# Optimization experiments

Measured on AMD Instinct MI355X. Metric: run time of the kernel, lower is better.

Reference implementation:

```python
import jax, jax.numpy as jnp
import numpy as np

D_MODEL = 1024
N_HEADS = 16
HEAD_DIM = D_MODEL // N_HEADS


def setup_inputs() -> dict:
    key = jax.random.key(0)
    k1, k2, k3 = jax.random.split(key, 3)
    x = jax.random.normal(k1, (2, 2048, D_MODEL), dtype=jnp.float32)
    w_qkv = jax.random.normal(k2, (3 * D_MODEL, D_MODEL), dtype=jnp.float32) * 0.02
    w_out = jax.random.normal(k3, (D_MODEL, D_MODEL), dtype=jnp.float32) * 0.02
    return {"x": x, "w_qkv": w_qkv, "w_out": w_out}


def reference(x, w_qkv, w_out):
    B, T, D = x.shape
    H, Hd = N_HEADS, HEAD_DIM
    # QKV projection: Linear stores weight as [out, in] -> '...i,oi->...o'
    qkv = jnp.einsum('bti,oi->bto', x, w_qkv)              # [B, T, 3D]
    # split (3*H, Hs) group-major, chunk into q/k/v of H heads each
    qkv = qkv.reshape(B, T, 3, H, Hd)
    q = jnp.transpose(qkv[:, :, 0], (0, 2, 1, 3))          # [B, H, T, Hd]
    k = jnp.transpose(qkv[:, :, 1], (0, 2, 1, 3))
    v = jnp.transpose(qkv[:, :, 2], (0, 2, 1, 3))
    scale = 1.0 / jnp.sqrt(jnp.asarray(Hd, dtype=x.dtype))
    scores = jnp.einsum('bhqd,bhkd->bhqk', q, k) * scale   # [B, H, T, T]
    causal = jnp.tril(jnp.ones((T, T), dtype=bool))        # [T, T]
    scores = jnp.where(causal[None, None], scores, jnp.asarray(-jnp.inf, dtype=scores.dtype))
    attn = jax.nn.softmax(scores, axis=-1)
    ctx = jnp.einsum('bhqk,bhkd->bhqd', attn, v)           # [B, H, T, Hd]
    ctx = jnp.transpose(ctx, (0, 2, 1, 3)).reshape(B, T, D)
    return jnp.einsum('bti,oi->bto', ctx, w_out)
```

## Files before the change

### kernel.cpp

```cpp
#include <hip/hip_runtime.h>


typedef short short8 __attribute__((ext_vector_type(8)));
typedef float f32x4 __attribute__((ext_vector_type(4)));
typedef unsigned short u16;
typedef unsigned int u32;

#define T_SEQ 2048
#define N_B 2
#define N_H 16
#define HD 64
#define DM 1024
#define TRIPLE 3072

__device__ __forceinline__ u16 f2bf(float f) {
  union { float f; unsigned u; } v;
  v.f = f;
  unsigned r = v.u + 0x7fffu + ((v.u >> 16) & 1u);
  return (u16)(r >> 16);
}

__device__ __forceinline__ float bf2f(u16 x) {
  return __uint_as_float((u32)x << 16);
}

__device__ __forceinline__ u32 cvtpk(float a, float b) {
  u32 r;
  asm("v_cvt_pk_bf16_f32 %0, %1, %2" : "=v"(r) : "v"(a), "v"(b));
  return r;
}

typedef const __attribute__((address_space(1))) void gvoid;
typedef __attribute__((address_space(3))) void lvoid;

__device__ __forceinline__ void g2l16(const void* g, void* l) {
  __builtin_amdgcn_global_load_lds((gvoid*)g, (lvoid*)l, 16, 0, 0);
}

__device__ __forceinline__ void storeC(float* p, float v) { *p = v; }
__device__ __forceinline__ void storeC(u16* p, float v) { *p = f2bf(v); }

__global__ __launch_bounds__(256) void cast_all(const float4* __restrict__ x,
                                                const float4* __restrict__ wq,
                                                const float4* __restrict__ wo,
                                                ushort4* __restrict__ out) {
  int i = blockIdx.x * 256 + threadIdx.x;
  const float4* src;
  int off;
  if (i < 1048576) { src = x; off = 0; }
  else if (i < 1835008) { src = wq; off = 1048576; }
  else { src = wo; off = 1835008; }
  float4 v = src[i - off];
  ushort4 o;
  o.x = f2bf(v.x); o.y = f2bf(v.y); o.z = f2bf(v.z); o.w = f2bf(v.w);
  out[i] = o;
}

__global__ __launch_bounds__(256) void vtrans(const u16* __restrict__ qkv,
                                              u16* __restrict__ vT) {
  const int tid = threadIdx.x;
  const int w = tid >> 6, lane = tid & 63;
  const int ti = lane >> 3, di = lane & 7;
  const int h = blockIdx.y, b = blockIdx.z;
  const int t0 = blockIdx.x * 256 + w * 64 + ti * 8;

  const u16* src = qkv + (size_t)(b * T_SEQ + t0) * TRIPLE + 2 * DM + h * HD + di * 8;
  u32 x[8][4];
#pragma unroll
  for (int e = 0; e < 8; ++e) {
    union { short8 v; u32 u[4]; } cv;
    cv.v = *(const short8*)(src + (size_t)e * TRIPLE);
#pragma unroll
    for (int j = 0; j < 4; ++j) x[e][j] = cv.u[j];
  }
  u32 y[8][4];
#pragma unroll
  for (int a = 0; a < 4; ++a)
#pragma unroll
    for (int j = 0; j < 4; ++j) {
      u32 lo = x[2 * a][j], hi = x[2 * a + 1][j];
      y[2 * a][j] = (lo & 0x0000FFFFu) | (hi << 16);
      y[2 * a + 1][j] = (lo >> 16) | (hi & 0xFFFF0000u);
    }
  u16* dst = vT + ((size_t)(b * N_H + h) * HD + di * 8) * T_SEQ + t0;
#pragma unroll
  for (int dd = 0; dd < 8; ++dd) {
    union { short8 v; u32 u[4]; } cv;
#pragma unroll
    for (int a = 0; a < 4; ++a) cv.u[a] = y[2 * a + (dd & 1)][dd >> 1];
    *(short8*)(dst + (size_t)dd * T_SEQ) = cv.v;
  }
}

template <typename OutT>
__global__ __launch_bounds__(512, 2) void gemm_bt_256(const u16* __restrict__ A,
                                                      const u16* __restrict__ W,
                                                      OutT* __restrict__ C,
                                                      int M, int N, int K) {
  __shared__ char As[2][32768];
  __shared__ char Bs[2][32768];

  const int tid = threadIdx.x;
  const int lane = tid & 63, w = tid >> 6;
  const int l15 = lane & 15, l4 = lane >> 4;
  const int wm = w >> 2, wn = w & 3;
  const int m0 = blockIdx.y * 256, n0 = blockIdx.x * 256;

  const int srow = tid >> 3;
  const int sswz = ((tid & 7) ^ (srow & 7)) << 3;
  const u16* Abase = A + (size_t)(m0 + srow) * K + sswz;
  const u16* Bbase = W + (size_t)(n0 + srow) * K + sswz;

  const f32x4 zero = {0.f, 0.f, 0.f, 0.f};
  f32x4 acc[8][4];
#pragma unroll
  for (int am = 0; am < 8; ++am)
#pragma unroll
    for (int n = 0; n < 4; ++n) acc[am][n] = zero;

#define STAGE8(k0_, buf_)                                                      \
  {                                                                            \
    _Pragma("unroll") for (int r_ = 0; r_ < 4; ++r_) {                         \
      g2l16(Abase + (size_t)(64 * r_) * K + (k0_),                             \
            As[buf_] + (r_ * 512 + tid) * 16);                                 \
      g2l16(Bbase + (size_t)(64 * r_) * K + (k0_),                             \
            Bs[buf_] + (r_ * 512 + tid) * 16);                                 \
    }                                                                          \
  }

  STAGE8(0, 0);

  const int nkt = K >> 6;
  for (int kt = 0;; ++kt) {
    const int cur = kt & 1;

    if (kt + 1 < nkt) {
      STAGE8((kt + 1) << 6, cur ^ 1);
      asm volatile("s_waitcnt vmcnt(8)" ::: "memory");
    } else {
      asm volatile("s_waitcnt vmcnt(0)" ::: "memory");
    }
    __builtin_amdgcn_s_barrier();

#pragma unroll
    for (int ph = 0; ph < 4; ++ph) {
      const int kk = ph >> 1, mh = ph & 1;
      short8 a[4], b[4];
#pragma unroll
      for (int m = 0; m < 4; ++m) {
        int row = wm * 128 + mh * 64 + m * 16 + l15;
        int slot = (kk * 4 + l4) ^ (row & 7);
        a[m] = *(const short8*)(As[cur] + row * 128 + slot * 16);
      }
#pragma unroll
      for (int n = 0; n < 4; ++n) {
        int row = wn * 64 + n * 16 + l15;
        int slot = (kk * 4 + l4) ^ (row & 7);
        b[n] = *(const short8*)(Bs[cur] + row * 128 + slot * 16);
      }
      asm volatile("s_waitcnt lgkmcnt(0)" ::: "memory");
      __builtin_amdgcn_s_setprio(1);
#pragma unroll
      for (int m = 0; m < 4; ++m)
#pragma unroll
        for (int n = 0; n < 4; ++n)
          acc[mh * 4 + m][n] =
              __builtin_amdgcn_mfma_f32_16x16x32_bf16(a[m], b[n], acc[mh * 4 + m][n], 0, 0, 0);
      __builtin_amdgcn_s_setprio(0);
    }

    if (kt + 1 >= nkt) break;
    __builtin_amdgcn_s_barrier();
  }
#undef STAGE8

#pragma unroll
  for (int am = 0; am < 8; ++am)
#pragma unroll
    for (int n = 0; n < 4; ++n)
#pragma unroll
      for (int r = 0; r < 4; ++r) {
        int row = m0 + wm * 128 + (am >> 2) * 64 + (am & 3) * 16 + l4 * 4 + r;
        int col = n0 + wn * 64 + n * 16 + l15;
        storeC(C + (size_t)row * N + col, acc[am][n][r]);
      }
}

template <typename OutT>
__global__ __launch_bounds__(256) void gemm_bt(const u16* __restrict__ A,
                                               const u16* __restrict__ W,
                                               OutT* __restrict__ C,
                                               int M, int N, int K) {
  __shared__ char As[128 * 64 * 2];
  __shared__ char Bs[128 * 64 * 2];
  const int tid = threadIdx.x;
  const int lane = tid & 63, w = tid >> 6;
  const int l15 = lane & 15, l4 = lane >> 4;
  const int m0 = blockIdx.y * 128, n0 = blockIdx.x * 128;
  const int wr = (w >> 1) * 64, wc = (w & 1) * 64;

  const f32x4 zero = {0.f, 0.f, 0.f, 0.f};
  f32x4 acc[4][4];
#pragma unroll
  for (int m = 0; m < 4; ++m)
#pragma unroll
    for (int n = 0; n < 4; ++n) acc[m][n] = zero;

  for (int k0 = 0; k0 < K; k0 += 64) {
#pragma unroll
    for (int i = 0; i < 4; ++i) {
      const int cb = (i * 4 + w) * 64;
      const int c = cb + lane;
      const int row = c >> 3;
      const int ks = ((c & 7) ^ (row & 7)) * 8;
      g2l16(A + (size_t)(m0 + row) * K + k0 + ks, As + (size_t)cb * 16);
      g2l16(W + (size_t)(n0 + row) * K + k0 + ks, Bs + (size_t)cb * 16);
    }
    __syncthreads();

#pragma unroll
    for (int kk = 0; kk < 2; ++kk) {
      short8 a[4], b[4];
#pragma unroll
      for (int m = 0; m < 4; ++m) {
        int row = wr + m * 16 + l15;
        int slot = (kk * 4 + l4) ^ (row & 7);
        a[m] = *(const short8*)(As + row * 128 + slot * 16);
      }
#pragma unroll
      for (int n = 0; n < 4; ++n) {
        int row = wc + n * 16 + l15;
        int slot = (kk * 4 + l4) ^ (row & 7);
        b[n] = *(const short8*)(Bs + row * 128 + slot * 16);
      }
#pragma unroll
      for (int m = 0; m < 4; ++m)
#pragma unroll
        for (int n = 0; n < 4; ++n)
          acc[m][n] = __builtin_amdgcn_mfma_f32_16x16x32_bf16(a[m], b[n], acc[m][n], 0, 0, 0);
    }
    __syncthreads();
  }

#pragma unroll
  for (int m = 0; m < 4; ++m)
#pragma unroll
    for (int n = 0; n < 4; ++n)
#pragma unroll
      for (int r = 0; r < 4; ++r) {
        int row = m0 + wr + m * 16 + l4 * 4 + r;
        int col = n0 + wc + n * 16 + l15;
        storeC(C + (size_t)row * N + col, acc[m][n][r]);
      }
}

__global__ __launch_bounds__(512) void attn_fwd(const u16* __restrict__ qkv,
                                                const u16* __restrict__ vT,
                                                u16* __restrict__ ctx) {
  __shared__ char Ks[3][8192];
  __shared__ char Vs[3][8192];
  __shared__ char Pl[8][2048];

  const int tid = threadIdx.x;
  const int lane = tid & 63, w = tid >> 6;
  const int l15 = lane & 15, l4 = lane >> 4;
  const int g = blockIdx.x;
  const int p = blockIdx.y;
  const int h = g & 15, b = g >> 4;
  const int q0A = 128 * p, q0B = 128 * (15 - p);
  const int nA = 2 * p + 2;

  const float c_log2 = 0.18033688011112042f;
  short8 qa2[2][2];
#pragma unroll
  for (int ps = 0; ps < 2; ++ps) {
    const int qq0 = ps ? q0B : q0A;
    const u16* qp = qkv + (size_t)(b * T_SEQ + qq0 + w * 16 + l15) * TRIPLE + h * HD;
#pragma unroll
    for (int kk = 0; kk < 2; ++kk) {
      short8 raw = *(const short8*)(qp + kk * 32 + l4 * 8);
      union { short8 v; u32 w4[4]; } qq;
#pragma unroll
      for (int j = 0; j < 4; ++j)
        qq.w4[j] = cvtpk(bf2f((u16)raw[2 * j]) * c_log2,
                         bf2f((u16)raw[2 * j + 1]) * c_log2);
      qa2[ps][kk] = qq.v;
    }
  }

  const int r0 = tid >> 3, c0 = tid & 7;
  const int swz = (c0 ^ (r0 & 7)) << 3;
  const u16* kbase = qkv + (size_t)(b * T_SEQ + r0) * TRIPLE + DM + h * HD + swz;
  const u16* vbase = vT + ((size_t)g * HD + r0) * T_SEQ + swz;

#define STAGE(kt_, buf_)                                                     \
  {                                                                          \
    g2l16(kbase + (size_t)((kt_) * (64 * TRIPLE)), Ks[buf_] + tid * 16);     \
    g2l16(vbase + (u32)((kt_) * 64), Vs[buf_] + tid * 16);                   \
  }

  char* Plb = Pl[w];

  const f32x4 zero = {0.f, 0.f, 0.f, 0.f};
  f32x4 o[4];
#pragma unroll
  for (int nt = 0; nt < 4; ++nt) o[nt] = zero;
  float mr = -INFINITY, lr = 0.f;
  short8 qa0 = qa2[0][0], qa1 = qa2[0][1];
  int q0 = q0A;

  STAGE(0, 0);
  STAGE(1, 1);
  asm volatile("s_waitcnt vmcnt(2)\n\ts_barrier" ::: "memory");

  int cur = 0;
  for (int i = 0;; ++i) {
    const int kt = (i < nA) ? i : 33 - i;

    if (i + 2 < 34) {
      const int kt2 = (i + 2 < nA) ? (i + 2) : 31 - i;
      int sb = cur - 1;
      if (sb < 0) sb = 2;
      STAGE(kt2, sb);
    }

    const int k0 = kt * 64;
    if (k0 <= q0 + w * 16) {
      f32x4 s[4];
#pragma unroll
      for (int mt = 0; mt < 4; ++mt) s[mt] = zero;
      __builtin_amdgcn_s_setprio(1);
#pragma unroll
      for (int mt = 0; mt < 4; ++mt) {
        int row = mt * 16 + l15;
        int slot0 = l4 ^ (row & 7);
        short8 kb0 = *(const short8*)(Ks[cur] + row * 128 + slot0 * 16);
        s[mt] = __builtin_amdgcn_mfma_f32_16x16x32_bf16(kb0, qa0, s[mt], 0, 0, 0);
        int slot1 = (4 + l4) ^ (row & 7);
        short8 kb1 = *(const short8*)(Ks[cur] + row * 128 + slot1 * 16);
        s[mt] = __builtin_amdgcn_mfma_f32_16x16x32_bf16(kb1, qa1, s[mt], 0, 0, 0);
      }
      __builtin_amdgcn_s_setprio(0);

      if (i >= nA - 2 && i <= nA + 1) {
        const int qrow = q0 + w * 16 + l15;
#pragma unroll
        for (int mt = 0; mt < 4; ++mt)
#pragma unroll
          for (int r = 0; r < 4; ++r) {
            int key = k0 + mt * 16 + l4 * 4 + r;
            if (key > qrow) s[mt][r] = -INFINITY;
          }
      }

      float mx = fmaxf(fmaxf(fmaxf(s[0][0], s[0][1]), fmaxf(s[0][2], s[0][3])),
                       fmaxf(fmaxf(s[1][0], s[1][1]), fmaxf(s[1][2], s[1][3])));
      mx = fmaxf(mx, fmaxf(fmaxf(fmaxf(s[2][0], s[2][1]), fmaxf(s[2][2], s[2][3])),
                           fmaxf(fmaxf(s[3][0], s[3][1]), fmaxf(s[3][2], s[3][3]))));
      mx = fmaxf(mx, __shfl_xor(mx, 16));
      mx = fmaxf(mx, __shfl_xor(mx, 32));
      if (!__all(mx - mr <= 8.0f)) {
        float mn = fmaxf(mr, mx);
        float fr = exp2f(mr - mn);
        lr *= fr;
#pragma unroll
        for (int r = 0; r < 4; ++r) {
          float frq = __shfl(fr, l4 * 4 + r);
#pragma unroll
          for (int nt = 0; nt < 4; ++nt) o[nt][r] *= frq;
        }
        mr = mn;
      }
      float ps = 0.f;
#pragma unroll
      for (int mt = 0; mt < 4; ++mt)
#pragma unroll
        for (int r = 0; r < 4; ++r) {
          float pv = exp2f(s[mt][r] - mr);
          s[mt][r] = pv;
          ps += pv;
        }
      lr += ps;

#pragma unroll
      for (int mt = 0; mt < 4; ++mt) {
        uint2 pw;
        pw.x = cvtpk(s[mt][0], s[mt][1]);
        pw.y = cvtpk(s[mt][2], s[mt][3]);
        int slot = ((mt * 2 + (l4 >> 1)) ^ (l15 & 7));
        *(uint2*)(Plb + l15 * 128 + (slot << 4) + ((l4 & 1) << 3)) = pw;
      }

      __builtin_amdgcn_s_setprio(1);
#pragma unroll
      for (int kk = 0; kk < 2; ++kk) {
        short8 pa = *(const short8*)(Plb + l15 * 128 + (((kk * 4 + l4) ^ (l15 & 7)) << 4));
#pragma unroll
        for (int nt = 0; nt < 4; ++nt) {
          int d = nt * 16 + l15;
          int slot = (kk * 4 + l4) ^ (l15 & 7);
          short8 vb = *(const short8*)(Vs[cur] + d * 128 + slot * 16);
          o[nt] = __builtin_amdgcn_mfma_f32_16x16x32_bf16(pa, vb, o[nt], 0, 0, 0);
        }
      }
      __builtin_amdgcn_s_setprio(0);
    }

    if (i == nA - 1 || i == 33) {
      lr += __shfl_xor(lr, 16);
      lr += __shfl_xor(lr, 32);
#pragma unroll
      for (int r = 0; r < 4; ++r) {
        float lrq = __shfl(lr, l4 * 4 + r);
        float inv = __builtin_amdgcn_rcpf(lrq);
        size_t t = (size_t)(b * T_SEQ + q0 + w * 16 + l4 * 4 + r);
#pragma unroll
        for (int nt = 0; nt < 4; ++nt)
          ctx[t * DM + h * HD + nt * 16 + l15] = f2bf(o[nt][r] * inv);
      }
      if (i == 33) break;
#pragma unroll
      for (int nt = 0; nt < 4; ++nt) o[nt] = zero;
      mr = -INFINITY; lr = 0.f;
      qa0 = qa2[1][0]; qa1 = qa2[1][1];
      q0 = q0B;
    }

    if (i == 32)
      asm volatile("s_waitcnt vmcnt(0)\n\ts_barrier" ::: "memory");
    else
      asm volatile("s_waitcnt vmcnt(2)\n\ts_barrier" ::: "memory");
    cur = (cur == 2) ? 0 : cur + 1;
  }
#undef STAGE
}

extern "C" void kernel_launch(void* const* d_in, const int* in_sizes, int n_in,
                              void* d_out, int out_size, void* d_ws, size_t ws_size,
                              hipStream_t stream) {
  const float* x = (const float*)d_in[0];
  const float* wqkv = (const float*)d_in[1];
  const float* wout = (const float*)d_in[2];
  float* out = (float*)d_out;
  char* ws = (char*)d_ws;

  u16* xb    = (u16*)(ws);
  u16* wqkvb = (u16*)(ws + 8u * 1024 * 1024);
  u16* woutb = (u16*)(ws + 14u * 1024 * 1024);
  u16* qkvb  = (u16*)(ws + 16u * 1024 * 1024);
  u16* ctxb  = (u16*)(ws + 40u * 1024 * 1024);
  u16* vTb   = (u16*)(ws + 48u * 1024 * 1024);

  cast_all<<<8192, 256, 0, stream>>>((const float4*)x, (const float4*)wqkv,
                                     (const float4*)wout, (ushort4*)xb);

  gemm_bt_256<u16><<<dim3(12, 16), 512, 0, stream>>>(xb, wqkvb, qkvb, 4096, 3072, 1024);

  vtrans<<<dim3(8, N_H, N_B), 256, 0, stream>>>(qkvb, vTb);

  attn_fwd<<<dim3(32, 8), 512, 0, stream>>>(qkvb, vTb, ctxb);

  gemm_bt<float><<<dim3(8, 32), 256, 0, stream>>>(ctxb, woutb, out, 4096, 1024, 1024);
}
```

Baseline: 129.9 us.

## Split GEMM K-tile into half-stages interleaved with MFMA phases

Reorganizes the 256x256 GEMM's shared-memory staging into four half-tiles (A/B × two K halves of 32), each loaded with a new XOR swizzle. The next tile's loads are issued piecewise inside each MFMA phase, with a finer-grained vmcnt wait and a barrier per phase. The aim is to spread global-to-LDS traffic across the compute phases instead of issuing it all in one burst. It adds two barriers per phase, which raises sync overhead, and it relies on a new swizzle whose bank-conflict behavior is unverified.

```diff
diff --git a/kernel.cpp b/kernel.cpp
--- a/kernel.cpp
+++ b/kernel.cpp
@@ -97,8 +97,7 @@
                                                       const u16* __restrict__ W,
                                                       OutT* __restrict__ C,
                                                       int M, int N, int K) {
-  __shared__ char As[2][32768];
-  __shared__ char Bs[2][32768];
+  __shared__ char Ls[2][2][2][16384];
 
   const int tid = threadIdx.x;
   const int lane = tid & 63, w = tid >> 6;
@@ -106,10 +105,26 @@
   const int wm = w >> 2, wn = w & 3;
   const int m0 = blockIdx.y * 256, n0 = blockIdx.x * 256;
 
-  const int srow = tid >> 3;
-  const int sswz = ((tid & 7) ^ (srow & 7)) << 3;
-  const u16* Abase = A + (size_t)(m0 + srow) * K + sswz;
-  const u16* Bbase = W + (size_t)(n0 + srow) * K + sswz;
+  const int c0 = tid, c1 = 512 + tid;
+  const int r0 = c0 >> 2, r1 = c1 >> 2;
+  const int k0off = ((c0 & 3) ^ (((r0 >> 1) ^ (r0 >> 3)) & 3)) << 3;
+  const int k1off = ((c1 & 3) ^ (((r1 >> 1) ^ (r1 >> 3)) & 3)) << 3;
+  const u16* A0 = A + (size_t)(m0 + r0) * K + k0off;
+  const u16* A1 = A + (size_t)(m0 + r1) * K + k1off;
+  const u16* B0 = W + (size_t)(n0 + r0) * K + k0off;
+  const u16* B1 = W + (size_t)(n0 + r1) * K + k1off;
+
+#define STAGEH(mat_, kh_, kt_, buf_)                                           \
+  {                                                                            \
+    const int ko_ = (kt_) * 64 + (kh_) * 32;                                   \
+    if ((mat_) == 0) {                                                         \
+      g2l16(A0 + ko_, Ls[buf_][0][kh_] + tid * 16);                            \
+      g2l16(A1 + ko_, Ls[buf_][0][kh_] + (512 + tid) * 16);                    \
+    } else {                                                                   \
+      g2l16(B0 + ko_, Ls[buf_][1][kh_] + tid * 16);                            \
+      g2l16(B1 + ko_, Ls[buf_][1][kh_] + (512 + tid) * 16);                    \
+    }                                                                          \
+  }
 
   const f32x4 zero = {0.f, 0.f, 0.f, 0.f};
   f32x4 acc[8][4];
@@ -118,47 +133,47 @@
 #pragma unroll
     for (int n = 0; n < 4; ++n) acc[am][n] = zero;
 
-#define STAGE8(k0_, buf_)                                                      \
-  {                                                                            \
-    _Pragma("unroll") for (int r_ = 0; r_ < 4; ++r_) {                         \
-      g2l16(Abase + (size_t)(64 * r_) * K + (k0_),                             \
-            As[buf_] + (r_ * 512 + tid) * 16);                                 \
-      g2l16(Bbase + (size_t)(64 * r_) * K + (k0_),                             \
-            Bs[buf_] + (r_ * 512 + tid) * 16);                                 \
-    }                                                                          \
-  }
-
-  STAGE8(0, 0);
-
   const int nkt = K >> 6;
-  for (int kt = 0;; ++kt) {
+
+  STAGEH(0, 0, 0, 0);
+  STAGEH(1, 0, 0, 0);
+  STAGEH(0, 1, 0, 0);
+  STAGEH(1, 1, 0, 0);
+  asm volatile("s_waitcnt vmcnt(4)" ::: "memory");
+  __builtin_amdgcn_s_barrier();
+
+  for (int kt = 0; kt < nkt; ++kt) {
     const int cur = kt & 1;
-
-    if (kt + 1 < nkt) {
-      STAGE8((kt + 1) << 6, cur ^ 1);
-      asm volatile("s_waitcnt vmcnt(8)" ::: "memory");
-    } else {
-      asm volatile("s_waitcnt vmcnt(0)" ::: "memory");
-    }
-    __builtin_amdgcn_s_barrier();
+    const bool notlast = (kt + 1 < nkt);
 
 #pragma unroll
     for (int ph = 0; ph < 4; ++ph) {
       const int kk = ph >> 1, mh = ph & 1;
+
       short8 a[4], b[4];
 #pragma unroll
       for (int m = 0; m < 4; ++m) {
         int row = wm * 128 + mh * 64 + m * 16 + l15;
-        int slot = (kk * 4 + l4) ^ (row & 7);
-        a[m] = *(const short8*)(As[cur] + row * 128 + slot * 16);
+        int slot = l4 ^ (((row >> 1) ^ (row >> 3)) & 3);
+        a[m] = *(const short8*)(Ls[cur][0][kk] + row * 64 + (slot << 4));
       }
 #pragma unroll
       for (int n = 0; n < 4; ++n) {
         int row = wn * 64 + n * 16 + l15;
-        int slot = (kk * 4 + l4) ^ (row & 7);
-        b[n] = *(const short8*)(Bs[cur] + row * 128 + slot * 16);
-      }
+        int slot = l4 ^ (((row >> 1) ^ (row >> 3)) & 3);
+        b[n] = *(const short8*)(Ls[cur][1][kk] + row * 64 + (slot << 4));
+      }
+
+      if (notlast) {
+        STAGEH(ph & 1, ph >> 1, kt + 1, cur ^ 1);
+        if (ph & 1) asm volatile("s_waitcnt vmcnt(4)" ::: "memory");
+      } else {
+        if (ph == 1) asm volatile("s_waitcnt vmcnt(0)" ::: "memory");
+      }
+      __builtin_amdgcn_s_barrier();
       asm volatile("s_waitcnt lgkmcnt(0)" ::: "memory");
+      __builtin_amdgcn_sched_barrier(0);
+
       __builtin_amdgcn_s_setprio(1);
 #pragma unroll
       for (int m = 0; m < 4; ++m)
@@ -167,12 +182,10 @@
           acc[mh * 4 + m][n] =
               __builtin_amdgcn_mfma_f32_16x16x32_bf16(a[m], b[n], acc[mh * 4 + m][n], 0, 0, 0);
       __builtin_amdgcn_s_setprio(0);
-    }
-
-    if (kt + 1 >= nkt) break;
-    __builtin_amdgcn_s_barrier();
-  }
-#undef STAGE8
+      __builtin_amdgcn_s_barrier();
+    }
+  }
+#undef STAGEH
 
 #pragma unroll
   for (int am = 0; am < 8; ++am)
```

Measured after the change: 133.6 us. +2.9%, slower.
